# Optimization experiments

Measured on AMD Instinct MI355X. Metric: run time of the kernel, lower is better.

## Reference

```python
import jax, jax.numpy as jnp
import numpy as np

B, N, D, H, T, DFF, OUT = 32, 256, 512, 8, 60, 2048, 2
EPS = 1e-5


def _mha(q, k, v, Wq, Wk, Wv, Wo, bq, bk, bv, bo):
    # torch nn.MultiheadAttention (batch_first): x @ W.T + b projections
    Bq, Lq, Dm = q.shape
    dh = Dm // H
    scale = 1.0 / np.sqrt(dh).astype(np.float32)
    qh = (q @ Wq.T + bq).reshape(Bq, Lq, H, dh).transpose(0, 2, 1, 3)
    kh = (k @ Wk.T + bk).reshape(Bq, k.shape[1], H, dh).transpose(0, 2, 1, 3)
    vh = (v @ Wv.T + bv).reshape(Bq, v.shape[1], H, dh).transpose(0, 2, 1, 3)
    a = jax.nn.softmax(jnp.einsum('bhqd,bhkd->bhqk', qh, kh) * scale, axis=-1)
    o = jnp.einsum('bhqk,bhkd->bhqd', a, vh).transpose(0, 2, 1, 3).reshape(Bq, Lq, Dm)
    return o @ Wo.T + bo


def _ln(x, w, b):
    m = x.mean(-1, keepdims=True)
    v = ((x - m) ** 2).mean(-1, keepdims=True)
    return (x - m) / jnp.sqrt(v + EPS) * w + b


def setup_inputs() -> dict:
    key = jax.random.key(0)
    ks = iter(jax.random.split(key, 64))

    def rn(shape, s=0.05):
        return jax.random.normal(next(ks), shape, dtype=jnp.float32) * s

    inp = {
        'H_v_all': rn((B, N, D), 1.0),
        'H_v0_init': rn((B, 1, 1, D), 1.0),
        'pe': rn((1, T, D), 1.0),  # positional_encoding parameter
    }
    # s_* : spatial_attn;  sa_* : decoder self-attn;  ca_* : decoder cross-attn
    for p in ('s', 'sa', 'ca'):
        for m in ('Wq', 'Wk', 'Wv', 'Wo'):
            inp[f'{p}_{m}'] = rn((D, D))
        for m in ('bq', 'bk', 'bv', 'bo'):
            inp[f'{p}_{m}'] = jnp.zeros((D,), jnp.float32)
    for i in (1, 2, 3):
        inp[f'ln{i}_w'] = jnp.ones((D,), jnp.float32)
        inp[f'ln{i}_b'] = jnp.zeros((D,), jnp.float32)
    inp['W1'] = rn((DFF, D)); inp['b1'] = jnp.zeros((DFF,), jnp.float32)
    inp['W2'] = rn((D, DFF)); inp['b2'] = jnp.zeros((D,), jnp.float32)
    inp['Wout'] = rn((OUT, D)); inp['bout'] = jnp.zeros((OUT,), jnp.float32)
    return inp


def reference(H_v_all, H_v0_init, pe,
              s_Wq, s_Wk, s_Wv, s_Wo, s_bq, s_bk, s_bv, s_bo,
              sa_Wq, sa_Wk, sa_Wv, sa_Wo, sa_bq, sa_bk, sa_bv, sa_bo,
              ca_Wq, ca_Wk, ca_Wv, ca_Wo, ca_bq, ca_bk, ca_bv, ca_bo,
              ln1_w, ln1_b, ln2_w, ln2_b, ln3_w, ln3_b,
              W1, b1, W2, b2, Wout, bout):

    def dec_layer(x, mem):
        # post-norm TransformerDecoderLayer, no masks (non-causal), relu FFN, eval (no dropout)
        sa = _mha(x, x, x, sa_Wq, sa_Wk, sa_Wv, sa_Wo, sa_bq, sa_bk, sa_bv, sa_bo)
        x = _ln(x + sa, ln1_w, ln1_b)
        ca = _mha(x, mem, mem, ca_Wq, ca_Wk, ca_Wv, ca_Wo, ca_bq, ca_bk, ca_bv, ca_bo)
        x = _ln(x + ca, ln2_w, ln2_b)
        ff = jax.nn.relu(x @ W1.T + b1) @ W2.T + b2
        return _ln(x + ff, ln3_w, ln3_b)

    tgt = H_v0_init  # (B, 1, 1, D), grows along dim 2
    outputs = []
    for t in range(T):
        tgt_pe = tgt + pe[:, :t + 1][:, None]        # (B,1,t+1,D)
        tgt_step = tgt_pe.reshape(B, t + 1, D)
        ctx = _mha(tgt_step[:, -1:, :], H_v_all, H_v_all,
                   s_Wq, s_Wk, s_Wv, s_Wo, s_bq, s_bk, s_bv, s_bo)
        decoded = dec_layer(tgt_step, H_v_all)
        nxt = decoded[:, -1:, :] + ctx               # (B,1,D)
        tgt = jnp.concatenate([tgt, nxt[:, None]], axis=2)
        outputs.append(nxt[:, None])                 # (B,1,1,D)
    out_seq = jnp.concatenate(outputs, axis=2)       # (B,1,T,D)
    return out_seq @ Wout.T + bout                   # (B,1,T,2)
```

## Files before the change

### kernel.cpp

```cpp
#include <hip/hip_runtime.h>


#define NB 32
#define NN 256
#define DD 512
#define NH 8
#define DH 64
#define TT 60
#define DF 2048
#define NBLK 256
#define NTHR 512

typedef unsigned short ushort_t;
typedef _Float16 half2v __attribute__((ext_vector_type(2)));

constexpr size_t SZ_KV  = (size_t)NB * NN * DD;
constexpr size_t SZ_ROW = (size_t)NB * DD;
constexpr size_t SZ_PAR = (size_t)NB * NH * DD;
constexpr size_t OFF_KS32 = 0;
constexpr size_t OFF_VS32 = SZ_KV;
constexpr size_t OFF_KC32 = 2 * SZ_KV;
constexpr size_t OFF_VC32 = 3 * SZ_KV;
constexpr size_t OFF_X    = 0;
constexpr size_t OFF_U1P  = OFF_X   + SZ_ROW;
constexpr size_t OFF_U2P  = OFF_U1P + SZ_PAR;
constexpr size_t OFF_U3P  = OFF_U2P + SZ_PAR;
constexpr size_t OFF_CTP0 = OFF_U3P + SZ_PAR;
constexpr size_t OFF_CTP1 = OFF_CTP0 + SZ_PAR;
constexpr size_t OFF_BF   = 4 * SZ_KV;
constexpr size_t UOFF_KST = 0;
constexpr size_t UOFF_KCT = SZ_KV;
constexpr size_t UOFF_VSH = 2 * SZ_KV;
constexpr size_t UOFF_VCH = 3 * SZ_KV;
constexpr size_t UOFF_W8  = 4 * SZ_KV;
constexpr size_t UOFF_W1  = UOFF_W8 + 8ull * DD * DD;
constexpr size_t UOFF_W2  = UOFF_W1 + (size_t)DD * DF;
constexpr size_t UEND     = UOFF_W2 + (size_t)DF * DD;
constexpr size_t OFF_FLG  = OFF_BF + (UEND + 1) / 2;

constexpr unsigned DYN_LDS = 131072;

__device__ __forceinline__ float ldg_a(const float* p) {
  return __hip_atomic_load(p, __ATOMIC_RELAXED, __HIP_MEMORY_SCOPE_AGENT);
}
__device__ __forceinline__ unsigned ldg_u(const unsigned* p) {
  return __hip_atomic_load(p, __ATOMIC_RELAXED, __HIP_MEMORY_SCOPE_AGENT);
}
__device__ __forceinline__ void stg_u(unsigned* p, unsigned v) {
  __hip_atomic_store(p, v, __ATOMIC_RELAXED, __HIP_MEMORY_SCOPE_AGENT);
}
__device__ __forceinline__ unsigned f2pk(float a, float b) {
  return __builtin_bit_cast(unsigned, __builtin_amdgcn_cvt_pkrtz(a, b));
}
__device__ __forceinline__ ushort_t f2h(float a) {
  return (ushort_t)(f2pk(a, 0.f) & 0xffffu);
}
__device__ __forceinline__ float h2f(ushort_t u) {
  return (float)__builtin_bit_cast(_Float16, u);
}
__device__ __forceinline__ float fdot2u(unsigned a, unsigned b, float c) {
  return __builtin_amdgcn_fdot2(__builtin_bit_cast(half2v, a),
                                __builtin_bit_cast(half2v, b), c, false);
}

struct Params {
  const float *pe;
  const float *sa_bq, *sa_bk, *sa_bv, *s_bq, *sa_bo, *s_bo, *ca_bq, *ca_bo;
  const float *ln1w, *ln1b, *ln2w, *ln2b, *ln3w, *ln3b;
  const float *b1, *b2, *Wout, *bout;
  const ushort_t *w8, *w1b, *w2b;
  const ushort_t *KsT, *KcT, *VsH, *VcH;
  float *xcur;
  unsigned *u1w, *u2w, *u3w, *ct0w, *ct1w;
  float *out;
  unsigned *flags;
};

__device__ __forceinline__ void set_flag(unsigned* fl, int tid, int h,
                                         unsigned val) {
  __builtin_amdgcn_s_waitcnt(0);
  __syncthreads();
  if (tid == 0)
    __hip_atomic_store(&fl[h], val, __ATOMIC_RELAXED,
                       __HIP_MEMORY_SCOPE_AGENT);
}
__device__ __forceinline__ void wait_ge(unsigned* fl, int tid,
                                        unsigned target) {
  if (tid < 64) {
    bool wait = true;
    while (wait) {
      unsigned v = target;
      if (tid < 8)
        v = __hip_atomic_load(&fl[tid], __ATOMIC_RELAXED,
                              __HIP_MEMORY_SCOPE_AGENT);
      wait = __any(v < target);
    }
  }
  __syncthreads();
}

#define SLAB_STORE(basep, val)                                         \
  {                                                                    \
    float _pv = __shfl_xor((val), 1);                                  \
    if (!(tid & 1)) stg_u((basep) + (tid >> 1), f2pk((val), _pv));     \
  }

__global__ __launch_bounds__(512) void decode_persistent(Params P) {
  __shared__ __align__(16) float sX[2048];
  __shared__ __align__(16) float sPart[512];
  __shared__ float sAux[64];
  __shared__ __align__(16) unsigned xh[256];
  __shared__ __align__(16) unsigned ph[384];
  __shared__ __align__(16) ushort_t cacheK[TT * 78];
  __shared__ __align__(16) ushort_t cacheV[TT * 64];
  extern __shared__ __align__(16) unsigned dynLds[];
  unsigned* Ks_l = dynLds;
  unsigned* Kc_l = dynLds + 8192;
  ushort_t* Vs_l = (ushort_t*)(dynLds + 16384);
  ushort_t* Vc_l = Vs_l + 16384;

  int tid = threadIdx.x;
  int bid = blockIdx.x;
  int b = bid >> 3, h = bid & 7;
  int idx8 = bid;
  unsigned* fl = P.flags + b * 64;
  int sel = tid & 1;

  {
    const uint4* gks = (const uint4*)((const unsigned*)P.KsT +
                       (((size_t)b * DD + h * DH) >> 1) * NN);
    const uint4* gkc = (const uint4*)((const unsigned*)P.KcT +
                       (((size_t)b * DD + h * DH) >> 1) * NN);
    const uint4* gvs = (const uint4*)(P.VsH + (size_t)idx8 * NN * DH);
    const uint4* gvc = (const uint4*)(P.VcH + (size_t)idx8 * NN * DH);
    uint4* dks = (uint4*)Ks_l;
    uint4* dkc = (uint4*)Kc_l;
    uint4* dvs = (uint4*)Vs_l;
    uint4* dvc = (uint4*)Vc_l;
    #pragma unroll
    for (int i = 0; i < 4; i++) {
      int idx = i * NTHR + tid;
      dks[idx] = gks[idx];
      dkc[idx] = gkc[idx];
      dvs[idx] = gvs[idx];
      dvc[idx] = gvc[idx];
    }
  }

  float x_f = ldg_a(P.xcur + (size_t)b * DD + tid);
  {
    float px = __shfl_xor(x_f, 1);
    if (!(tid & 1)) xh[tid >> 1] = f2pk(x_f, px);
  }
  __syncthreads();

  for (int t = 0; t < TT; t++) {
    {
      {
        int w = tid >> 6, c = tid & 63, m = w >> 1, half = w & 1;
        int col = h * DH + c;
        const uint2* wp = (const uint2*)(P.w8 + (size_t)m * DD * DD) + col;
        float acc = 0.f;
        #pragma unroll 8
        for (int kq = half * 64; kq < half * 64 + 64; kq++) {
          uint2 wv = wp[(size_t)kq * DD];
          uint2 xv = *(const uint2*)&xh[kq * 2];
          acc = fdot2u(wv.x, xv.x, acc);
          acc = fdot2u(wv.y, xv.y, acc);
        }
        sPart[tid] = acc;
      }
      __syncthreads();
      if (tid < 256) {
        int m = tid >> 6, c = tid & 63, col = h * DH + c;
        const float* bias = (m == 0) ? P.sa_bq : (m == 1) ? P.sa_bk
                          : (m == 2) ? P.sa_bv : P.s_bq;
        float val = sPart[(2 * m) * 64 + c] + sPart[(2 * m + 1) * 64 + c]
                    + bias[col];
        sX[512 + tid] = val;
        if (m == 1) cacheK[t * 78 + c] = f2h(val);
        if (m == 2) cacheV[t * 64 + c] = f2h(val);
      }
      __syncthreads();

      int L = t + 1;
      float* sQ  = sX + 512;
      float* sQs = sX + 704;
      float* sPb = sX + 768;
      if (tid < 64) {
        float e = 0.f;
        if (tid < L) {
          const unsigned* kl = (const unsigned*)(cacheK + (size_t)tid * 78);
          float a = 0.f;
          #pragma unroll 8
          for (int i = 0; i < 32; i++) {
            unsigned w = kl[i];
            a += sQ[2 * i] * h2f((ushort_t)(w & 0xffffu)) +
                 sQ[2 * i + 1] * h2f((ushort_t)(w >> 16));
          }
          e = __expf(a * 0.125f);
        }
        float s2 = e;
        #pragma unroll
        for (int s = 32; s >= 1; s >>= 1) s2 += __shfl_xor(s2, s);
        sPb[tid] = e * (1.f / s2);
        float o = 0.f;
        for (int j = 0; j < L; j++)
          o += sPb[j] * h2f(cacheV[j * 64 + tid]);
        float po = __shfl_xor(o, 1);
        if (!(tid & 1)) ph[32 + (tid >> 1)] = f2pk(o, po);
      } else if (tid < 320) {
        int n = tid - 64;
        float a = 0.f;
        #pragma unroll 8
        for (int i = 0; i < 32; i++) {
          unsigned w = Ks_l[i * NN + n];
          a += sQs[2 * i] * h2f((ushort_t)(w & 0xffffu)) +
               sQs[2 * i + 1] * h2f((ushort_t)(w >> 16));
        }
        sPart[n] = a * 0.125f;
      }
      __syncthreads();
      {
        unsigned* u1w = P.u1w + ((size_t)b * NH + h) * 256;
        const uint2* wpa = (const uint2*)(P.w8 + 4ull * DD * DD) + tid;
        float acc1 = (h == 0) ? P.sa_bo[tid] + x_f : 0.f;
        #pragma unroll 8
        for (int j = 0; j < 16; j++) {
          int k4 = h * 16 + j;
          uint2 wv = wpa[(size_t)k4 * DD];
          uint2 x1 = *(const uint2*)&ph[32 + 2 * j];
          acc1 = fdot2u(wv.x, x1.x, acc1);
          acc1 = fdot2u(wv.y, x1.y, acc1);
        }
        SLAB_STORE(u1w, acc1);
      }
      set_flag(fl, tid, h, 3 * t + 1);
      float* sPr = sX + 1536;
      if (tid < 256) {
        float e = __expf(sPart[tid]);
        sPr[tid] = e;
        int w = tid >> 6;
        float s2 = e;
        #pragma unroll
        for (int s = 32; s >= 1; s >>= 1) s2 += __shfl_xor(s2, s);
        if ((tid & 63) == 0) sAux[4 + w] = s2;
      }
      __syncthreads();
      float* sB = sX + 1024;
      {
        int g = tid >> 6, d = tid & 63;
        float inv = 1.f / (sAux[4] + sAux[5] + sAux[6] + sAux[7]);
        const ushort_t* vp = Vs_l + (g * 32) * DH + d;
        float acc = 0.f;
        #pragma unroll 4
        for (int n = 0; n < 32; n++) acc += sPr[g * 32 + n] * h2f(vp[n * DH]);
        sB[tid] = acc * inv;
      }
      __syncthreads();
      if (tid < 64) {
        float o = 0.f;
        #pragma unroll
        for (int i = 0; i < 8; i++) o += sB[i * 64 + tid];
        float po = __shfl_xor(o, 1);
        if (!(tid & 1)) ph[64 + (tid >> 1)] = f2pk(o, po);
      }
      __syncthreads();
      {
        unsigned* ctw = ((t & 1) ? P.ct1w : P.ct0w) + ((size_t)b * NH + h) * 256;
        const uint2* wpb = (const uint2*)(P.w8 + 5ull * DD * DD) + tid;
        float acc2 = (h == 0) ? P.s_bo[tid] : 0.f;
        #pragma unroll 8
        for (int j = 0; j < 16; j++) {
          int k4 = h * 16 + j;
          uint2 wv2 = wpb[(size_t)k4 * DD];
          uint2 x2 = *(const uint2*)&ph[64 + 2 * j];
          acc2 = fdot2u(wv2.x, x2.x, acc2);
          acc2 = fdot2u(wv2.y, x2.y, acc2);
        }
        SLAB_STORE(ctw, acc2);
      }
    }

    float y1f;
    {
      wait_ge(fl, tid, 3 * t + 1);
      float u = 0.f;
      {
        const unsigned* pp = P.u1w + (size_t)b * NH * 256 + (tid >> 1);
        #pragma unroll
        for (int i = 0; i < 8; i++) {
          unsigned w = ldg_u(pp + i * 256);
          u += h2f((ushort_t)(sel ? (w >> 16) : (w & 0xffffu)));
        }
      }
      {
        int w = tid >> 6;
        float s = u, q2 = u * u;
        #pragma unroll
        for (int m = 32; m >= 1; m >>= 1) { s += __shfl_xor(s, m); q2 += __shfl_xor(q2, m); }
        if ((tid & 63) == 0) { sAux[w] = s; sAux[8 + w] = q2; }
      }
      __syncthreads();
      {
        float ss = 0.f, qq = 0.f;
        #pragma unroll
        for (int i = 0; i < 8; i++) { ss += sAux[i]; qq += sAux[8 + i]; }
        float mean = ss * (1.f / 512.f);
        float inv = rsqrtf(qq * (1.f / 512.f) - mean * mean + 1e-5f);
        y1f = (u - mean) * inv * P.ln1w[tid] + P.ln1b[tid];
        float py = __shfl_xor(y1f, 1);
        if (!(tid & 1)) ph[128 + (tid >> 1)] = f2pk(y1f, py);
      }
      __syncthreads();
      {
        int c = tid & 63, w = tid >> 6, col = h * DH + c;
        const uint2* wp = (const uint2*)(P.w8 + 6ull * DD * DD) + col;
        float acc = 0.f;
        #pragma unroll 8
        for (int kq = w * 16; kq < w * 16 + 16; kq++) {
          uint2 wv = wp[(size_t)kq * DD];
          uint2 xv = *(const uint2*)&ph[128 + 2 * kq];
          acc = fdot2u(wv.x, xv.x, acc);
          acc = fdot2u(wv.y, xv.y, acc);
        }
        sPart[tid] = acc;
      }
      __syncthreads();
      if (tid < 64) {
        float o = 0.f;
        #pragma unroll
        for (int i = 0; i < 8; i++) o += sPart[i * 64 + tid];
        o += P.ca_bq[h * DH + tid];
        float po = __shfl_xor(o, 1);
        if (!(tid & 1)) ph[tid >> 1] = f2pk(o, po);
      }
      __syncthreads();
      {
        int n = tid & 255, dh2 = tid >> 8;
        float a = 0.f;
        #pragma unroll 8
        for (int dw = dh2 * 16; dw < dh2 * 16 + 16; dw++)
          a = fdot2u(Kc_l[dw * NN + n], ph[dw], a);
        sPart[tid] = a;
      }
      __syncthreads();
      float* sPr = sX + 1536;
      if (tid < 256) {
        float e = __expf((sPart[tid] + sPart[256 + tid]) * 0.125f);
        sPr[tid] = e;
        int w = tid >> 6;
        float s2 = e;
        #pragma unroll
        for (int s = 32; s >= 1; s >>= 1) s2 += __shfl_xor(s2, s);
        if ((tid & 63) == 0) sAux[4 + w] = s2;
      }
      __syncthreads();
      float* sB = sX + 1024;
      {
        int g = tid >> 6, d = tid & 63;
        float inv = 1.f / (sAux[4] + sAux[5] + sAux[6] + sAux[7]);
        const ushort_t* vp = Vc_l + (g * 32) * DH + d;
        float acc = 0.f;
        #pragma unroll 4
        for (int n = 0; n < 32; n++) acc += sPr[g * 32 + n] * h2f(vp[n * DH]);
        sB[tid] = acc * inv;
      }
      __syncthreads();
      if (tid < 64) {
        float o = 0.f;
        #pragma unroll
        for (int i = 0; i < 8; i++) o += sB[i * 64 + tid];
        float po = __shfl_xor(o, 1);
        if (!(tid & 1)) ph[32 + (tid >> 1)] = f2pk(o, po);
      }
      __syncthreads();
      {
        const uint2* wp = (const uint2*)(P.w8 + 7ull * DD * DD) + tid;
        float acc = (h == 0) ? P.ca_bo[tid] + y1f : 0.f;
        #pragma unroll 8
        for (int j = 0; j < 16; j++) {
          int k4 = h * 16 + j;
          uint2 wv = wp[(size_t)k4 * DD];
          uint2 xv = *(const uint2*)&ph[32 + 2 * j];
          acc = fdot2u(wv.x, xv.x, acc);
          acc = fdot2u(wv.y, xv.y, acc);
        }
        unsigned* u2w = P.u2w + ((size_t)b * NH + h) * 256;
        SLAB_STORE(u2w, acc);
      }
    }
    set_flag(fl, tid, h, 3 * t + 2);

    float zf;
    {
      wait_ge(fl, tid, 3 * t + 2);
      float v = 0.f;
      {
        const unsigned* pp = P.u2w + (size_t)b * NH * 256 + (tid >> 1);
        #pragma unroll
        for (int i = 0; i < 8; i++) {
          unsigned w = ldg_u(pp + i * 256);
          v += h2f((ushort_t)(sel ? (w >> 16) : (w & 0xffffu)));
        }
      }
      {
        int w = tid >> 6;
        float s = v, q2 = v * v;
        #pragma unroll
        for (int m = 32; m >= 1; m >>= 1) { s += __shfl_xor(s, m); q2 += __shfl_xor(q2, m); }
        if ((tid & 63) == 0) { sAux[w] = s; sAux[8 + w] = q2; }
      }
      __syncthreads();
      {
        float ss = 0.f, qq = 0.f;
        #pragma unroll
        for (int i = 0; i < 8; i++) { ss += sAux[i]; qq += sAux[8 + i]; }
        float mean = ss * (1.f / 512.f);
        float inv = rsqrtf(qq * (1.f / 512.f) - mean * mean + 1e-5f);
        zf = (v - mean) * inv * P.ln2w[tid] + P.ln2b[tid];
        float pz = __shfl_xor(zf, 1);
        if (!(tid & 1)) ph[128 + (tid >> 1)] = f2pk(zf, pz);
      }
      __syncthreads();
      {
        int c = tid & 255, half = tid >> 8, col = h * 256 + c;
        const uint2* wp = (const uint2*)P.w1b + col;
        float acc = 0.f;
        #pragma unroll 8
        for (int kq = half * 64; kq < half * 64 + 64; kq++) {
          uint2 wv = wp[(size_t)kq * DF];
          uint2 xv = *(const uint2*)&ph[128 + 2 * kq];
          acc = fdot2u(wv.x, xv.x, acc);
          acc = fdot2u(wv.y, xv.y, acc);
        }
        sPart[tid] = acc;
      }
      __syncthreads();
      if (tid < 256) {
        float hv = fmaxf(sPart[tid] + sPart[256 + tid] + P.b1[h * 256 + tid], 0.f);
        float pv = __shfl_xor(hv, 1);
        if (!(tid & 1)) ph[tid >> 1] = f2pk(hv, pv);
      }
      __syncthreads();
      {
        const uint2* wp = (const uint2*)P.w2b + tid;
        float acc = (h == 0) ? zf + P.b2[tid] : 0.f;
        #pragma unroll 8
        for (int j = 0; j < 64; j++) {
          int k4 = h * 64 + j;
          uint2 wv = wp[(size_t)k4 * DD];
          uint2 xv = *(const uint2*)&ph[2 * j];
          acc = fdot2u(wv.x, xv.x, acc);
          acc = fdot2u(wv.y, xv.y, acc);
        }
        unsigned* u3w = P.u3w + ((size_t)b * NH + h) * 256;
        SLAB_STORE(u3w, acc);
      }
    }
    set_flag(fl, tid, h, 3 * t + 3);

    {
      wait_ge(fl, tid, 3 * t + 3);
      float u = 0.f, ctxv = 0.f;
      {
        const unsigned* pp = P.u3w + (size_t)b * NH * 256 + (tid >> 1);
        const unsigned* cp = ((t & 1) ? P.ct1w : P.ct0w)
                             + (size_t)b * NH * 256 + (tid >> 1);
        #pragma unroll
        for (int i = 0; i < 8; i++) {
          unsigned w1 = ldg_u(pp + i * 256);
          unsigned w2 = ldg_u(cp + i * 256);
          u    += h2f((ushort_t)(sel ? (w1 >> 16) : (w1 & 0xffffu)));
          ctxv += h2f((ushort_t)(sel ? (w2 >> 16) : (w2 & 0xffffu)));
        }
      }
      {
        int w = tid >> 6;
        float s = u, q2 = u * u;
        #pragma unroll
        for (int m = 32; m >= 1; m >>= 1) { s += __shfl_xor(s, m); q2 += __shfl_xor(q2, m); }
        if ((tid & 63) == 0) { sAux[w] = s; sAux[8 + w] = q2; }
      }
      __syncthreads();
      float ss = 0.f, qq = 0.f;
      #pragma unroll
      for (int i = 0; i < 8; i++) { ss += sAux[i]; qq += sAux[8 + i]; }
      float mean = ss * (1.f / 512.f);
      float inv = rsqrtf(qq * (1.f / 512.f) - mean * mean + 1e-5f);
      float nxt = (u - mean) * inv * P.ln3w[tid] + P.ln3b[tid] + ctxv;
      float p = (t < TT - 1) ? P.pe[(size_t)(t + 1) * DD + tid] : 0.f;
      x_f = nxt + p;
      {
        float px = __shfl_xor(x_f, 1);
        if (!(tid & 1)) xh[tid >> 1] = f2pk(x_f, px);
      }
      if (h == 0) sX[tid] = nxt;
      __syncthreads();
      if (h == 0) {
        {
          int c = tid >> 8, l = tid & 255;
          float a = sX[l] * P.Wout[(size_t)c * DD + l] +
                    sX[l + 256] * P.Wout[(size_t)c * DD + l + 256];
          #pragma unroll
          for (int m = 32; m >= 1; m >>= 1) a += __shfl_xor(a, m);
          if ((tid & 63) == 0) sAux[16 + (tid >> 6)] = a;
        }
        __syncthreads();
        if (tid == 0)
          P.out[((size_t)b * TT + t) * 2 + 0] =
              sAux[16] + sAux[17] + sAux[18] + sAux[19] + P.bout[0];
        if (tid == 256)
          P.out[((size_t)b * TT + t) * 2 + 1] =
              sAux[20] + sAux[21] + sAux[22] + sAux[23] + P.bout[1];
      }
      __syncthreads();
    }
  }
}

__global__ __launch_bounds__(256) void gemm_kv(
    const float* __restrict__ A,
    const float* __restrict__ W0, const float* __restrict__ W1_,
    const float* __restrict__ W2_, const float* __restrict__ W3_,
    const float* __restrict__ b0, const float* __restrict__ b1_,
    const float* __restrict__ b2_, const float* __restrict__ b3_,
    float* __restrict__ O0, float* __restrict__ O1,
    float* __restrict__ O2, float* __restrict__ O3) {
  __shared__ __align__(16) float As[8][128];
  __shared__ __align__(16) float Bs[8][128];
  int tid = threadIdx.x;
  int bx = blockIdx.x, by = blockIdx.y;
  int mm = bx >> 2;
  int col0 = (bx & 3) * 128;
  const float* W = mm == 0 ? W0 : mm == 1 ? W1_ : mm == 2 ? W2_ : W3_;
  const float* bias = mm == 0 ? b0 : mm == 1 ? b1_ : mm == 2 ? b2_ : b3_;
  float* O = mm == 0 ? O0 : mm == 1 ? O1 : mm == 2 ? O2 : O3;
  int tx = tid & 15, ty = tid >> 4;
  int m0 = by * 128;
  int lr = tid >> 1, lk = (tid & 1) * 4;
  const float* Ap = A + (size_t)(m0 + lr) * DD + lk;
  const float* Wp = W + (size_t)(col0 + lr) * DD + lk;
  float c[8][8] = {};
  for (int k0 = 0; k0 < DD; k0 += 8) {
    float4 av = *(const float4*)(Ap + k0);
    float4 wv = *(const float4*)(Wp + k0);
    __syncthreads();
    As[lk + 0][lr] = av.x; As[lk + 1][lr] = av.y; As[lk + 2][lr] = av.z; As[lk + 3][lr] = av.w;
    Bs[lk + 0][lr] = wv.x; Bs[lk + 1][lr] = wv.y; Bs[lk + 2][lr] = wv.z; Bs[lk + 3][lr] = wv.w;
    __syncthreads();
    #pragma unroll
    for (int k = 0; k < 8; k++) {
      float a[8], bb[8];
      *(float4*)&a[0] = *(const float4*)&As[k][ty * 8];
      *(float4*)&a[4] = *(const float4*)&As[k][ty * 8 + 4];
      *(float4*)&bb[0] = *(const float4*)&Bs[k][tx * 8];
      *(float4*)&bb[4] = *(const float4*)&Bs[k][tx * 8 + 4];
      #pragma unroll
      for (int i = 0; i < 8; i++)
        #pragma unroll
        for (int j = 0; j < 8; j++) c[i][j] += a[i] * bb[j];
    }
  }
  const float* bp = bias + col0 + tx * 8;
  for (int i = 0; i < 8; i++) {
    int row = m0 + ty * 8 + i;
    float* op = O + (size_t)row * DD + col0 + tx * 8;
    #pragma unroll
    for (int jq = 0; jq < 8; jq += 4) {
      float4 v;
      v.x = c[i][jq + 0] + bp[jq + 0];
      v.y = c[i][jq + 1] + bp[jq + 1];
      v.z = c[i][jq + 2] + bp[jq + 2];
      v.w = c[i][jq + 3] + bp[jq + 3];
      *(float4*)(op + jq) = v;
    }
  }
}

__global__ __launch_bounds__(256) void pack_kT(const float* __restrict__ Ks32,
                                               const float* __restrict__ Kc32,
                                               ushort_t* __restrict__ KsT,
                                               ushort_t* __restrict__ KcT) {
  int z = blockIdx.z;
  int b = z >> 1;
  const float* in = ((z & 1) ? Kc32 : Ks32) + (size_t)b * NN * DD;
  ushort_t* out = ((z & 1) ? KcT : KsT) + (size_t)b * NN * DD;
  int r0 = blockIdx.x * 32, c0 = blockIdx.y * 32;
  __shared__ float tile[32][33];
  int tid = threadIdx.x;
  int i = tid >> 3, j4 = (tid & 7) * 4;
  float4 v = *(const float4*)(in + (size_t)(r0 + i) * DD + c0 + j4);
  tile[i][j4] = v.x; tile[i][j4 + 1] = v.y; tile[i][j4 + 2] = v.z; tile[i][j4 + 3] = v.w;
  __syncthreads();
  int d = c0 + i;
  ushort_t* op = out + (size_t)(d >> 1) * (2 * NN) + 2 * (r0 + j4) + (d & 1);
  op[0] = f2h(tile[j4][i]);     op[2] = f2h(tile[j4 + 1][i]);
  op[4] = f2h(tile[j4 + 2][i]); op[6] = f2h(tile[j4 + 3][i]);
}

__global__ __launch_bounds__(256) void pack_vh(const float* __restrict__ Vs32,
                                               const float* __restrict__ Vc32,
                                               ushort_t* __restrict__ VsH,
                                               ushort_t* __restrict__ VcH) {
  const float* src = blockIdx.y ? Vc32 : Vs32;
  ushort_t* dst = blockIdx.y ? VcH : VsH;
  size_t idx = (size_t)blockIdx.x * 1024 + threadIdx.x * 4;
  float4 v = *(const float4*)(src + idx);
  int d512 = (int)(idx & 511);
  int n = (int)((idx >> 9) & 255);
  int b = (int)(idx >> 17);
  int h = d512 >> 6, d = d512 & 63;
  ushort_t* op = dst + (((size_t)(b * 8 + h) * NN + n) * DH + d);
  op[0] = f2h(v.x); op[1] = f2h(v.y); op[2] = f2h(v.z); op[3] = f2h(v.w);
}

struct PWItem { const float* in; ushort_t* out; int C; int K; };
struct PWArgs { PWItem m[10]; };
__global__ __launch_bounds__(256) void pack_w(PWArgs a) {
  PWItem it = a.m[blockIdx.y];
  int total = it.C * (it.K >> 2);
  int e = blockIdx.x * 256 + threadIdx.x;
  if (e >= total) return;
  int kd = it.K >> 2;
  int k4 = e % kd, col = e / kd;
  float4 v = *(const float4*)(it.in + (size_t)col * it.K + k4 * 4);
  unsigned lo = f2pk(v.x, v.y), hi = f2pk(v.z, v.w);
  ushort4 o;
  o.x = (ushort_t)(lo & 0xffffu); o.y = (ushort_t)(lo >> 16);
  o.z = (ushort_t)(hi & 0xffffu); o.w = (ushort_t)(hi >> 16);
  *((ushort4*)it.out + (size_t)k4 * it.C + col) = o;
}

__global__ __launch_bounds__(256) void init_x(const float* __restrict__ hv0,
                                              const float* __restrict__ pe,
                                              float* __restrict__ ws,
                                              unsigned* __restrict__ flags) {
  int i = blockIdx.x * 256 + threadIdx.x;
  ws[OFF_X + i] = hv0[i] + pe[i & (DD - 1)];
  if (i < 2048) flags[i] = 0u;
}

extern "C" void kernel_launch(void* const* d_in, const int* in_sizes, int n_in,
                              void* d_out, int out_size, void* d_ws, size_t ws_size,
                              hipStream_t stream) {
  const float* H_v_all = (const float*)d_in[0];
  const float* H_v0    = (const float*)d_in[1];
  const float* pe      = (const float*)d_in[2];
  const float* s_Wq = (const float*)d_in[3];
  const float* s_Wk = (const float*)d_in[4];
  const float* s_Wv = (const float*)d_in[5];
  const float* s_Wo = (const float*)d_in[6];
  const float* s_bq = (const float*)d_in[7];
  const float* s_bk = (const float*)d_in[8];
  const float* s_bv = (const float*)d_in[9];
  const float* s_bo = (const float*)d_in[10];
  const float* sa_Wq = (const float*)d_in[11];
  const float* sa_Wk = (const float*)d_in[12];
  const float* sa_Wv = (const float*)d_in[13];
  const float* sa_Wo = (const float*)d_in[14];
  const float* sa_bq = (const float*)d_in[15];
  const float* sa_bk = (const float*)d_in[16];
  const float* sa_bv = (const float*)d_in[17];
  const float* sa_bo = (const float*)d_in[18];
  const float* ca_Wq = (const float*)d_in[19];
  const float* ca_Wk = (const float*)d_in[20];
  const float* ca_Wv = (const float*)d_in[21];
  const float* ca_Wo = (const float*)d_in[22];
  const float* ca_bq = (const float*)d_in[23];
  const float* ca_bk = (const float*)d_in[24];
  const float* ca_bv = (const float*)d_in[25];
  const float* ca_bo = (const float*)d_in[26];
  const float* ln1w = (const float*)d_in[27];
  const float* ln1b = (const float*)d_in[28];
  const float* ln2w = (const float*)d_in[29];
  const float* ln2b = (const float*)d_in[30];
  const float* ln3w = (const float*)d_in[31];
  const float* ln3b = (const float*)d_in[32];
  const float* W1   = (const float*)d_in[33];
  const float* b1   = (const float*)d_in[34];
  const float* W2   = (const float*)d_in[35];
  const float* b2   = (const float*)d_in[36];
  const float* Wout = (const float*)d_in[37];
  const float* bout = (const float*)d_in[38];

  float* ws = (float*)d_ws;
  float* Ks32 = ws + OFF_KS32;
  float* Vs32 = ws + OFF_VS32;
  float* Kc32 = ws + OFF_KC32;
  float* Vc32 = ws + OFF_VC32;
  ushort_t* ub = (ushort_t*)(ws + OFF_BF);
  unsigned* flags = (unsigned*)(ws + OFF_FLG);

  hipLaunchKernelGGL(gemm_kv, dim3(16, 64), dim3(256), 0, stream,
                     H_v_all, s_Wk, s_Wv, ca_Wk, ca_Wv,
                     s_bk, s_bv, ca_bk, ca_bv, Ks32, Vs32, Kc32, Vc32);

  hipLaunchKernelGGL(pack_kT, dim3(8, 16, 64), dim3(256), 0, stream,
                     Ks32, Kc32, ub + UOFF_KST, ub + UOFF_KCT);
  hipLaunchKernelGGL(pack_vh, dim3((unsigned)(SZ_KV / 1024), 2), dim3(256), 0,
                     stream, Vs32, Vc32, ub + UOFF_VSH, ub + UOFF_VCH);

  PWArgs pw;
  pw.m[0] = {sa_Wq, ub + UOFF_W8 + 0ull * DD * DD, DD, DD};
  pw.m[1] = {sa_Wk, ub + UOFF_W8 + 1ull * DD * DD, DD, DD};
  pw.m[2] = {sa_Wv, ub + UOFF_W8 + 2ull * DD * DD, DD, DD};
  pw.m[3] = {s_Wq,  ub + UOFF_W8 + 3ull * DD * DD, DD, DD};
  pw.m[4] = {sa_Wo, ub + UOFF_W8 + 4ull * DD * DD, DD, DD};
  pw.m[5] = {s_Wo,  ub + UOFF_W8 + 5ull * DD * DD, DD, DD};
  pw.m[6] = {ca_Wq, ub + UOFF_W8 + 6ull * DD * DD, DD, DD};
  pw.m[7] = {ca_Wo, ub + UOFF_W8 + 7ull * DD * DD, DD, DD};
  pw.m[8] = {W1, ub + UOFF_W1, DF, DD};
  pw.m[9] = {W2, ub + UOFF_W2, DD, DF};
  hipLaunchKernelGGL(pack_w, dim3(1024, 10), dim3(256), 0, stream, pw);

  hipLaunchKernelGGL(init_x, dim3(64), dim3(256), 0, stream,
                     H_v0, pe, ws, flags);

  static bool attr_set = false;
  if (!attr_set) {
    hipFuncSetAttribute((const void*)decode_persistent,
                        hipFuncAttributeMaxDynamicSharedMemorySize, DYN_LDS);
    attr_set = true;
  }

  Params P;
  P.pe = pe;
  P.sa_bq = sa_bq; P.sa_bk = sa_bk; P.sa_bv = sa_bv; P.s_bq = s_bq;
  P.sa_bo = sa_bo; P.s_bo = s_bo; P.ca_bq = ca_bq; P.ca_bo = ca_bo;
  P.ln1w = ln1w; P.ln1b = ln1b; P.ln2w = ln2w; P.ln2b = ln2b;
  P.ln3w = ln3w; P.ln3b = ln3b;
  P.b1 = b1; P.b2 = b2; P.Wout = Wout; P.bout = bout;
  P.w8 = ub + UOFF_W8; P.w1b = ub + UOFF_W1; P.w2b = ub + UOFF_W2;
  P.KsT = ub + UOFF_KST; P.KcT = ub + UOFF_KCT;
  P.VsH = ub + UOFF_VSH; P.VcH = ub + UOFF_VCH;
  P.xcur = ws + OFF_X;
  P.u1w = (unsigned*)(ws + OFF_U1P);
  P.u2w = (unsigned*)(ws + OFF_U2P);
  P.u3w = (unsigned*)(ws + OFF_U3P);
  P.ct0w = (unsigned*)(ws + OFF_CTP0);
  P.ct1w = (unsigned*)(ws + OFF_CTP1);
  P.out = (float*)d_out;
  P.flags = flags;

  void* kargs[] = { (void*)&P };
  hipLaunchCooperativeKernel((void*)decode_persistent, dim3(NBLK), dim3(NTHR),
                             kargs, DYN_LDS, stream);
}
```

Measured before the change: 2.107 ms.

## Double workgroup size to 1024 threads and split GEMV reductions further

Raises the persistent decode kernel from 512 to 1024 threads per block. Every matrix-vector product and attention reduction is split across twice as many threads, with an extra shared-memory partial-sum reduction and barrier added. The aim is more memory-level parallelism per block to hide weight-load latency. In exchange it adds barriers and idle threads in the 512-wide LayerNorm phases, and it raises register pressure, which can limit occupancy at 1024 threads.

Result: slower. 3.785 ms (+79.6%).

```diff
diff --git a/kernel.cpp b/kernel.cpp
--- a/kernel.cpp
+++ b/kernel.cpp
@@ -9,7 +9,7 @@
 #define TT 60
 #define DF 2048
 #define NBLK 256
-#define NTHR 512
+#define NTHR 1024
 
 typedef unsigned short ushort_t;
 typedef _Float16 half2v __attribute__((ext_vector_type(2)));
@@ -105,9 +105,9 @@
     if (!(tid & 1)) stg_u((basep) + (tid >> 1), f2pk((val), _pv));     \
   }
 
-__global__ __launch_bounds__(512) void decode_persistent(Params P) {
-  __shared__ __align__(16) float sX[2048];
-  __shared__ __align__(16) float sPart[512];
+__global__ __launch_bounds__(1024) void decode_persistent(Params P) {
+  __shared__ __align__(16) float sX[1792];
+  __shared__ __align__(16) float sPart[1024];
   __shared__ float sAux[64];
   __shared__ __align__(16) unsigned xh[256];
   __shared__ __align__(16) unsigned ph[384];
@@ -138,7 +138,7 @@
     uint4* dvs = (uint4*)Vs_l;
     uint4* dvc = (uint4*)Vc_l;
     #pragma unroll
-    for (int i = 0; i < 4; i++) {
+    for (int i = 0; i < 2; i++) {
       int idx = i * NTHR + tid;
       dks[idx] = gks[idx];
       dkc[idx] = gkc[idx];
@@ -147,8 +147,9 @@
     }
   }
 
-  float x_f = ldg_a(P.xcur + (size_t)b * DD + tid);
-  {
+  float x_f = 0.f;
+  if (tid < 512) {
+    x_f = ldg_a(P.xcur + (size_t)b * DD + tid);
     float px = __shfl_xor(x_f, 1);
     if (!(tid & 1)) xh[tid >> 1] = f2pk(x_f, px);
   }
@@ -157,12 +158,12 @@
   for (int t = 0; t < TT; t++) {
     {
       {
-        int w = tid >> 6, c = tid & 63, m = w >> 1, half = w & 1;
+        int w = tid >> 6, c = tid & 63, m = w >> 2, q = w & 3;
         int col = h * DH + c;
         const uint2* wp = (const uint2*)(P.w8 + (size_t)m * DD * DD) + col;
         float acc = 0.f;
         #pragma unroll 8
-        for (int kq = half * 64; kq < half * 64 + 64; kq++) {
+        for (int kq = q * 32; kq < q * 32 + 32; kq++) {
           uint2 wv = wp[(size_t)kq * DD];
           uint2 xv = *(const uint2*)&xh[kq * 2];
           acc = fdot2u(wv.x, xv.x, acc);
@@ -175,8 +176,9 @@
         int m = tid >> 6, c = tid & 63, col = h * DH + c;
         const float* bias = (m == 0) ? P.sa_bq : (m == 1) ? P.sa_bk
                           : (m == 2) ? P.sa_bv : P.s_bq;
-        float val = sPart[(2 * m) * 64 + c] + sPart[(2 * m + 1) * 64 + c]
-                    + bias[col];
+        float val = sPart[(m * 4 + 0) * 64 + c] + sPart[(m * 4 + 1) * 64 + c]
+                  + sPart[(m * 4 + 2) * 64 + c] + sPart[(m * 4 + 3) * 64 + c]
+                  + bias[col];
         sX[512 + tid] = val;
         if (m == 1) cacheK[t * 78 + c] = f2h(val);
         if (m == 2) cacheV[t * 64 + c] = f2h(val);
@@ -209,36 +211,43 @@
           o += sPb[j] * h2f(cacheV[j * 64 + tid]);
         float po = __shfl_xor(o, 1);
         if (!(tid & 1)) ph[32 + (tid >> 1)] = f2pk(o, po);
-      } else if (tid < 320) {
-        int n = tid - 64;
+      } else if (tid >= 512) {
+        int q = tid - 512, n = q & 255, dh2 = q >> 8;
         float a = 0.f;
         #pragma unroll 8
-        for (int i = 0; i < 32; i++) {
+        for (int i = dh2 * 16; i < dh2 * 16 + 16; i++) {
           unsigned w = Ks_l[i * NN + n];
           a += sQs[2 * i] * h2f((ushort_t)(w & 0xffffu)) +
                sQs[2 * i + 1] * h2f((ushort_t)(w >> 16));
         }
-        sPart[n] = a * 0.125f;
-      }
-      __syncthreads();
-      {
-        unsigned* u1w = P.u1w + ((size_t)b * NH + h) * 256;
-        const uint2* wpa = (const uint2*)(P.w8 + 4ull * DD * DD) + tid;
-        float acc1 = (h == 0) ? P.sa_bo[tid] + x_f : 0.f;
-        #pragma unroll 8
-        for (int j = 0; j < 16; j++) {
+        sPart[q] = a;
+      }
+      __syncthreads();
+      {
+        int o = tid & 511, jh = tid >> 9;
+        const uint2* wpa = (const uint2*)(P.w8 + 4ull * DD * DD) + o;
+        float acc1 = 0.f;
+        #pragma unroll 8
+        for (int j = jh * 8; j < jh * 8 + 8; j++) {
           int k4 = h * 16 + j;
           uint2 wv = wpa[(size_t)k4 * DD];
           uint2 x1 = *(const uint2*)&ph[32 + 2 * j];
           acc1 = fdot2u(wv.x, x1.x, acc1);
           acc1 = fdot2u(wv.y, x1.y, acc1);
         }
+        sX[tid] = acc1;
+      }
+      __syncthreads();
+      if (tid < 512) {
+        unsigned* u1w = P.u1w + ((size_t)b * NH + h) * 256;
+        float acc1 = sX[tid] + sX[512 + tid] +
+                     ((h == 0) ? P.sa_bo[tid] + x_f : 0.f);
         SLAB_STORE(u1w, acc1);
       }
       set_flag(fl, tid, h, 3 * t + 1);
       float* sPr = sX + 1536;
       if (tid < 256) {
-        float e = __expf(sPart[tid]);
+        float e = __expf((sPart[tid] + sPart[256 + tid]) * 0.125f);
         sPr[tid] = e;
         int w = tid >> 6;
         float s2 = e;
@@ -247,54 +256,59 @@
         if ((tid & 63) == 0) sAux[4 + w] = s2;
       }
       __syncthreads();
-      float* sB = sX + 1024;
+      float* sB = sX;
       {
         int g = tid >> 6, d = tid & 63;
         float inv = 1.f / (sAux[4] + sAux[5] + sAux[6] + sAux[7]);
-        const ushort_t* vp = Vs_l + (g * 32) * DH + d;
+        const ushort_t* vp = Vs_l + (g * 16) * DH + d;
         float acc = 0.f;
         #pragma unroll 4
-        for (int n = 0; n < 32; n++) acc += sPr[g * 32 + n] * h2f(vp[n * DH]);
+        for (int n = 0; n < 16; n++) acc += sPr[g * 16 + n] * h2f(vp[n * DH]);
         sB[tid] = acc * inv;
       }
       __syncthreads();
       if (tid < 64) {
         float o = 0.f;
         #pragma unroll
-        for (int i = 0; i < 8; i++) o += sB[i * 64 + tid];
+        for (int i = 0; i < 16; i++) o += sB[i * 64 + tid];
         float po = __shfl_xor(o, 1);
         if (!(tid & 1)) ph[64 + (tid >> 1)] = f2pk(o, po);
       }
       __syncthreads();
       {
-        unsigned* ctw = ((t & 1) ? P.ct1w : P.ct0w) + ((size_t)b * NH + h) * 256;
-        const uint2* wpb = (const uint2*)(P.w8 + 5ull * DD * DD) + tid;
-        float acc2 = (h == 0) ? P.s_bo[tid] : 0.f;
-        #pragma unroll 8
-        for (int j = 0; j < 16; j++) {
+        int o = tid & 511, jh = tid >> 9;
+        const uint2* wpb = (const uint2*)(P.w8 + 5ull * DD * DD) + o;
+        float acc2 = 0.f;
+        #pragma unroll 8
+        for (int j = jh * 8; j < jh * 8 + 8; j++) {
           int k4 = h * 16 + j;
           uint2 wv2 = wpb[(size_t)k4 * DD];
           uint2 x2 = *(const uint2*)&ph[64 + 2 * j];
           acc2 = fdot2u(wv2.x, x2.x, acc2);
           acc2 = fdot2u(wv2.y, x2.y, acc2);
         }
+        sPart[tid] = acc2;
+      }
+      __syncthreads();
+      if (tid < 512) {
+        unsigned* ctw = ((t & 1) ? P.ct1w : P.ct0w) + ((size_t)b * NH + h) * 256;
+        float acc2 = sPart[tid] + sPart[512 + tid] +
+                     ((h == 0) ? P.s_bo[tid] : 0.f);
         SLAB_STORE(ctw, acc2);
       }
     }
 
-    float y1f;
+    float y1f = 0.f;
     {
       wait_ge(fl, tid, 3 * t + 1);
       float u = 0.f;
-      {
+      if (tid < 512) {
         const unsigned* pp = P.u1w + (size_t)b * NH * 256 + (tid >> 1);
         #pragma unroll
         for (int i = 0; i < 8; i++) {
           unsigned w = ldg_u(pp + i * 256);
           u += h2f((ushort_t)(sel ? (w >> 16) : (w & 0xffffu)));
         }
-      }
-      {
         int w = tid >> 6;
         float s = u, q2 = u * u;
         #pragma unroll
@@ -302,7 +316,7 @@
         if ((tid & 63) == 0) { sAux[w] = s; sAux[8 + w] = q2; }
       }
       __syncthreads();
-      {
+      if (tid < 512) {
         float ss = 0.f, qq = 0.f;
         #pragma unroll
         for (int i = 0; i < 8; i++) { ss += sAux[i]; qq += sAux[8 + i]; }
@@ -318,7 +332,7 @@
         const uint2* wp = (const uint2*)(P.w8 + 6ull * DD * DD) + col;
         float acc = 0.f;
         #pragma unroll 8
-        for (int kq = w * 16; kq < w * 16 + 16; kq++) {
+        for (int kq = w * 8; kq < w * 8 + 8; kq++) {
           uint2 wv = wp[(size_t)kq * DD];
           uint2 xv = *(const uint2*)&ph[128 + 2 * kq];
           acc = fdot2u(wv.x, xv.x, acc);
@@ -330,24 +344,25 @@
       if (tid < 64) {
         float o = 0.f;
         #pragma unroll
-        for (int i = 0; i < 8; i++) o += sPart[i * 64 + tid];
+        for (int i = 0; i < 16; i++) o += sPart[i * 64 + tid];
         o += P.ca_bq[h * DH + tid];
         float po = __shfl_xor(o, 1);
         if (!(tid & 1)) ph[tid >> 1] = f2pk(o, po);
       }
       __syncthreads();
       {
-        int n = tid & 255, dh2 = tid >> 8;
+        int n = tid & 255, dh4 = tid >> 8;
         float a = 0.f;
         #pragma unroll 8
-        for (int dw = dh2 * 16; dw < dh2 * 16 + 16; dw++)
+        for (int dw = dh4 * 8; dw < dh4 * 8 + 8; dw++)
           a = fdot2u(Kc_l[dw * NN + n], ph[dw], a);
         sPart[tid] = a;
       }
       __syncthreads();
       float* sPr = sX + 1536;
       if (tid < 256) {
-        float e = __expf((sPart[tid] + sPart[256 + tid]) * 0.125f);
+        float e = __expf((sPart[tid] + sPart[256 + tid] +
+                          sPart[512 + tid] + sPart[768 + tid]) * 0.125f);
         sPr[tid] = e;
         int w = tid >> 6;
         float s2 = e;
@@ -356,55 +371,60 @@
         if ((tid & 63) == 0) sAux[4 + w] = s2;
       }
       __syncthreads();
-      float* sB = sX + 1024;
+      float* sB = sX;
       {
         int g = tid >> 6, d = tid & 63;
         float inv = 1.f / (sAux[4] + sAux[5] + sAux[6] + sAux[7]);
-        const ushort_t* vp = Vc_l + (g * 32) * DH + d;
+        const ushort_t* vp = Vc_l + (g * 16) * DH + d;
         float acc = 0.f;
         #pragma unroll 4
-        for (int n = 0; n < 32; n++) acc += sPr[g * 32 + n] * h2f(vp[n * DH]);
+        for (int n = 0; n < 16; n++) acc += sPr[g * 16 + n] * h2f(vp[n * DH]);
         sB[tid] = acc * inv;
       }
       __syncthreads();
       if (tid < 64) {
         float o = 0.f;
         #pragma unroll
-        for (int i = 0; i < 8; i++) o += sB[i * 64 + tid];
+        for (int i = 0; i < 16; i++) o += sB[i * 64 + tid];
         float po = __shfl_xor(o, 1);
         if (!(tid & 1)) ph[32 + (tid >> 1)] = f2pk(o, po);
       }
       __syncthreads();
       {
-        const uint2* wp = (const uint2*)(P.w8 + 7ull * DD * DD) + tid;
-        float acc = (h == 0) ? P.ca_bo[tid] + y1f : 0.f;
-        #pragma unroll 8
-        for (int j = 0; j < 16; j++) {
+        int o = tid & 511, jh = tid >> 9;
+        const uint2* wp = (const uint2*)(P.w8 + 7ull * DD * DD) + o;
+        float acc = 0.f;
+        #pragma unroll 8
+        for (int j = jh * 8; j < jh * 8 + 8; j++) {
           int k4 = h * 16 + j;
           uint2 wv = wp[(size_t)k4 * DD];
           uint2 xv = *(const uint2*)&ph[32 + 2 * j];
           acc = fdot2u(wv.x, xv.x, acc);
           acc = fdot2u(wv.y, xv.y, acc);
         }
+        sPart[tid] = acc;
+      }
+      __syncthreads();
+      if (tid < 512) {
         unsigned* u2w = P.u2w + ((size_t)b * NH + h) * 256;
+        float acc = sPart[tid] + sPart[512 + tid] +
+                    ((h == 0) ? P.ca_bo[tid] + y1f : 0.f);
         SLAB_STORE(u2w, acc);
       }
     }
     set_flag(fl, tid, h, 3 * t + 2);
 
-    float zf;
+    float zf = 0.f;
     {
       wait_ge(fl, tid, 3 * t + 2);
       float v = 0.f;
-      {
+      if (tid < 512) {
         const unsigned* pp = P.u2w + (size_t)b * NH * 256 + (tid >> 1);
         #pragma unroll
         for (int i = 0; i < 8; i++) {
           unsigned w = ldg_u(pp + i * 256);
           v += h2f((ushort_t)(sel ? (w >> 16) : (w & 0xffffu)));
         }
-      }
-      {
         int w = tid >> 6;
         float s = v, q2 = v * v;
         #pragma unroll
@@ -412,7 +432,7 @@
         if ((tid & 63) == 0) { sAux[w] = s; sAux[8 + w] = q2; }
       }
       __syncthreads();
-      {
+      if (tid < 512) {
         float ss = 0.f, qq = 0.f;
         #pragma unroll
         for (int i = 0; i < 8; i++) { ss += sAux[i]; qq += sAux[8 + i]; }
@@ -428,7 +448,7 @@
         const uint2* wp = (const uint2*)P.w1b + col;
         float acc = 0.f;
         #pragma unroll 8
-        for (int kq = half * 64; kq < half * 64 + 64; kq++) {
+        for (int kq = half * 32; kq < half * 32 + 32; kq++) {
           uint2 wv = wp[(size_t)kq * DF];
           uint2 xv = *(const uint2*)&ph[128 + 2 * kq];
           acc = fdot2u(wv.x, xv.x, acc);
@@ -438,23 +458,31 @@
       }
       __syncthreads();
       if (tid < 256) {
-        float hv = fmaxf(sPart[tid] + sPart[256 + tid] + P.b1[h * 256 + tid], 0.f);
+        float hv = fmaxf(sPart[tid] + sPart[256 + tid] + sPart[512 + tid] +
+                         sPart[768 + tid] + P.b1[h * 256 + tid], 0.f);
         float pv = __shfl_xor(hv, 1);
         if (!(tid & 1)) ph[tid >> 1] = f2pk(hv, pv);
       }
       __syncthreads();
       {
-        const uint2* wp = (const uint2*)P.w2b + tid;
-        float acc = (h == 0) ? zf + P.b2[tid] : 0.f;
-        #pragma unroll 8
-        for (int j = 0; j < 64; j++) {
+        int o = tid & 511, jh = tid >> 9;
+        const uint2* wp = (const uint2*)P.w2b + o;
+        float acc = 0.f;
+        #pragma unroll 8
+        for (int j = jh * 32; j < jh * 32 + 32; j++) {
           int k4 = h * 64 + j;
           uint2 wv = wp[(size_t)k4 * DD];
           uint2 xv = *(const uint2*)&ph[2 * j];
           acc = fdot2u(wv.x, xv.x, acc);
           acc = fdot2u(wv.y, xv.y, acc);
         }
+        sPart[tid] = acc;
+      }
+      __syncthreads();
+      if (tid < 512) {
         unsigned* u3w = P.u3w + ((size_t)b * NH + h) * 256;
+        float acc = sPart[tid] + sPart[512 + tid] +
+                    ((h == 0) ? zf + P.b2[tid] : 0.f);
         SLAB_STORE(u3w, acc);
       }
     }
@@ -463,7 +491,7 @@
     {
       wait_ge(fl, tid, 3 * t + 3);
       float u = 0.f, ctxv = 0.f;
-      {
+      if (tid < 512) {
         const unsigned* pp = P.u3w + (size_t)b * NH * 256 + (tid >> 1);
         const unsigned* cp = ((t & 1) ? P.ct1w : P.ct0w)
                              + (size_t)b * NH * 256 + (tid >> 1);
@@ -474,8 +502,6 @@
           u    += h2f((ushort_t)(sel ? (w1 >> 16) : (w1 & 0xffffu)));
           ctxv += h2f((ushort_t)(sel ? (w2 >> 16) : (w2 & 0xffffu)));
         }
-      }
-      {
         int w = tid >> 6;
         float s = u, q2 = u * u;
         #pragma unroll
@@ -483,22 +509,22 @@
         if ((tid & 63) == 0) { sAux[w] = s; sAux[8 + w] = q2; }
       }
       __syncthreads();
-      float ss = 0.f, qq = 0.f;
-      #pragma unroll
-      for (int i = 0; i < 8; i++) { ss += sAux[i]; qq += sAux[8 + i]; }
-      float mean = ss * (1.f / 512.f);
-      float inv = rsqrtf(qq * (1.f / 512.f) - mean * mean + 1e-5f);
-      float nxt = (u - mean) * inv * P.ln3w[tid] + P.ln3b[tid] + ctxv;
-      float p = (t < TT - 1) ? P.pe[(size_t)(t + 1) * DD + tid] : 0.f;
-      x_f = nxt + p;
-      {
+      if (tid < 512) {
+        float ss = 0.f, qq = 0.f;
+        #pragma unroll
+        for (int i = 0; i < 8; i++) { ss += sAux[i]; qq += sAux[8 + i]; }
+        float mean = ss * (1.f / 512.f);
+        float inv = rsqrtf(qq * (1.f / 512.f) - mean * mean + 1e-5f);
+        float nxt = (u - mean) * inv * P.ln3w[tid] + P.ln3b[tid] + ctxv;
+        float p = (t < TT - 1) ? P.pe[(size_t)(t + 1) * DD + tid] : 0.f;
+        x_f = nxt + p;
         float px = __shfl_xor(x_f, 1);
         if (!(tid & 1)) xh[tid >> 1] = f2pk(x_f, px);
-      }
-      if (h == 0) sX[tid] = nxt;
+        if (h == 0) sX[tid] = nxt;
+      }
       __syncthreads();
       if (h == 0) {
-        {
+        if (tid < 512) {
           int c = tid >> 8, l = tid & 255;
           float a = sX[l] * P.Wout[(size_t)c * DD + l] +
                     sX[l + 256] * P.Wout[(size_t)c * DD + l + 256];
```
